# Kernel tuning notes

Measured on AMD Instinct MI355X. Metric: run time of the kernel, lower is better.

## Reference

```python
import jax, jax.numpy as jnp
import numpy as np

NUM_HEADS = 16
HEAD_DIM = 64
HIDDEN = NUM_HEADS * HEAD_DIM  # 1024


def get_rel_pos(q_size, k_size, rel_pos):
    # q_size == k_size here and rel_pos already has 2*size-1 rows, so the
    # F.interpolate(mode='linear') resize in the original is an identity.
    # relative_coords = q - k + (k_size - 1)  (scale factors are 1.0)
    coords = jnp.arange(q_size)[:, None] - jnp.arange(k_size)[None, :] + (k_size - 1)
    return rel_pos[coords]  # [q_size, k_size, head_dim]


def setup_inputs() -> dict:
    key = jax.random.key(0)
    ks = jax.random.split(key, 7)
    B, H, W = 4, 56, 28
    inp = {
        "hidden_states": jax.random.normal(ks[0], (B, H, W, HIDDEN), jnp.float32),
        "qkv_w": jax.random.normal(ks[1], (3 * HIDDEN, HIDDEN), jnp.float32) * 0.02,
        "qkv_b": jax.random.normal(ks[2], (3 * HIDDEN,), jnp.float32) * 0.02,
        "proj_w": jax.random.normal(ks[3], (HIDDEN, HIDDEN), jnp.float32) * 0.02,
        "proj_b": jax.random.normal(ks[4], (HIDDEN,), jnp.float32) * 0.02,
        "rel_pos_h": jax.random.normal(ks[5], (2 * H - 1, HEAD_DIM), jnp.float32) * 0.02,
        "rel_pos_w": jax.random.normal(ks[6], (2 * W - 1, HEAD_DIM), jnp.float32) * 0.02,
    }
    return inp


def reference(hidden_states, qkv_w, qkv_b, proj_w, proj_b, rel_pos_h, rel_pos_w):
    B, H, W, C = hidden_states.shape
    N = H * W
    scale = HEAD_DIM ** -0.5

    # qkv projection -> [3, B*heads, N, head_dim]
    qkv = hidden_states @ qkv_w.T + qkv_b
    qkv = qkv.reshape(B, N, 3, NUM_HEADS, HEAD_DIM).transpose(2, 0, 3, 1, 4)
    qkv = qkv.reshape(3, B * NUM_HEADS, N, HEAD_DIM)
    query, key_, value = qkv[0], qkv[1], qkv[2]

    # scaled dot-product scores, fully materialized as in the original
    attn = jnp.einsum('bqd,bkd->bqk', query * scale, key_)  # [B*heads, N, N]

    # decomposed relative position bias
    Rh = get_rel_pos(H, H, rel_pos_h)  # [H, H, d]
    Rw = get_rel_pos(W, W, rel_pos_w)  # [W, W, d]
    q_r = query.reshape(B * NUM_HEADS, H, W, HEAD_DIM)
    rel_h = jnp.einsum('bhwc,hkc->bhwk', q_r, Rh)  # [B*heads, H, W, H]
    rel_w = jnp.einsum('bhwc,wkc->bhwk', q_r, Rw)  # [B*heads, H, W, W]
    attn = attn.reshape(B * NUM_HEADS, H, W, H, W)
    attn = attn + rel_h[:, :, :, :, None] + rel_w[:, :, :, None, :]
    attn = attn.reshape(B * NUM_HEADS, N, N)

    attn = jax.nn.softmax(attn.astype(jnp.float32), axis=-1).astype(query.dtype)

    out = jnp.einsum('bqk,bkd->bqd', attn, value)
    out = out.reshape(B, NUM_HEADS, H, W, HEAD_DIM).transpose(0, 2, 3, 1, 4)
    out = out.reshape(B, H, W, C)
    out = out @ proj_w.T + proj_b
    return out
```

## Files before the change

### kernel.cpp

```cpp
#include <hip/hip_runtime.h>
#include <hip/hip_bf16.h>
#include <stdint.h>

typedef __bf16 bf16;
typedef __bf16 bf16x2 __attribute__((ext_vector_type(2)));
typedef __bf16 bf16x4 __attribute__((ext_vector_type(4)));
typedef __bf16 bf16x8 __attribute__((ext_vector_type(8)));
typedef float f32x4 __attribute__((ext_vector_type(4)));

#define AS1 __attribute__((address_space(1)))
#define AS3 __attribute__((address_space(3)))

static __device__ __forceinline__ void async_cp16(const bf16* g, bf16* l) {
    __builtin_amdgcn_global_load_lds((const AS1 void*)g, (AS3 void*)l, 16, 0, 0);
}

static __device__ __forceinline__ bf16x4 cvt4(f32x4 v) {
    bf16x4 r;
    r[0] = (bf16)v[0]; r[1] = (bf16)v[1]; r[2] = (bf16)v[2]; r[3] = (bf16)v[3];
    return r;
}

static __device__ __forceinline__ float fast_exp2(float x) {
#if __has_builtin(__builtin_amdgcn_exp2f)
    return __builtin_amdgcn_exp2f(x);
#else
    return __expf(x * 0.69314718056f);
#endif
}

__global__ __launch_bounds__(256) void cvt_kernel(
    const float* __restrict__ src, bf16* __restrict__ dst, int n4) {
    int i = blockIdx.x * 256 + threadIdx.x;
    const int stride = gridDim.x * 256;
    for (; i < n4; i += stride)
        ((bf16x4*)dst)[i] = cvt4(((const f32x4*)src)[i]);
}

__global__ __launch_bounds__(256) void build_kone(bf16* __restrict__ Kone) {
    const int idx = blockIdx.x * 256 + threadIdx.x;
    if (idx >= 6400) return;
    const int key = idx >> 2, chunk = idx & 3;
    const int hk = key / 28;
    const int wk = key - hk * 28;
    const int kt = key >> 6;
    const int ha = (kt << 6) / 28;
    const int jw = 27 - wk;
    const int jh = 31 - (hk - ha);
    bf16x8 v;
#pragma unroll
    for (int e = 0; e < 8; e++) {
        const int j = chunk * 8 + e;
        v[e] = (j == jw || j == jh) ? (bf16)1.0f : (bf16)0.0f;
    }
    *(bf16x8*)&Kone[key * 32 + chunk * 8] = v;
}


#define QKV_EPILOGUE()                                                        \
    for (int nt = 0; nt < 4; nt++) {                                          \
        const int n_ = n0 + wn + nt * 16 + lm;                                \
        const float bv = bias[n_];                                            \
        const int s = n_ >> 10, rem = n_ & 1023;                              \
        const int h = rem >> 6, d = rem & 63;                                 \
        const float qsc = (s == 0) ? 0.18033688011112042f : 1.0f;             \
        for (int mt = 0; mt < 4; mt++) {                                      \
            for (int r = 0; r < 4; r++) {                                     \
                const int m_ = m0 + wm + mt * 16 + quad * 4 + r;              \
                const int b = m_ / 1568;                                      \
                const int pix = m_ - b * 1568;                                \
                const int g = b * 16 + h;                                     \
                const bf16 v = (bf16)((acc[mt][nt][r] + bv) * qsc);           \
                if (s == 0)      Qb[((size_t)g * 1568 + pix) * 64 + d] = v;   \
                else if (s == 1) Kb[((size_t)g * 1568 + pix) * 64 + d] = v;   \
                else {                                                        \
                    const int lk = pix & 31;                                  \
                    const int ppix = (pix & ~31) | ((lk & 15) << 1) | (lk >> 4); \
                    Vt[((size_t)g * 64 + d) * 1568 + ppix] = v;               \
                }                                                             \
            }                                                                 \
        }                                                                     \
    }

__global__ __launch_bounds__(256) void qkv_gemm_bf16(
    const bf16* __restrict__ A, const bf16* __restrict__ W,
    const float* __restrict__ bias, bf16* __restrict__ Qb,
    bf16* __restrict__ Kb, bf16* __restrict__ Vt) {
    __shared__ bf16 As[128 * 32];
    __shared__ bf16 Bs[128 * 32];
    const int t = threadIdx.x;
    const int wid = t >> 6, lane = t & 63;
    const int m0 = blockIdx.x * 128, n0 = blockIdx.y * 128;
    const int wm = (wid & 1) * 64, wn = (wid >> 1) * 64;
    const int r_i = lane >> 2, c8 = (lane & 3) * 8;
    const int lm = lane & 15, quad = lane >> 4;

    f32x4 acc[4][4] = {};
    for (int k0 = 0; k0 < 1024; k0 += 32) {
        __syncthreads();
        for (int i = 0; i < 2; i++) {
            const int blk = wid * 2 + i;
            async_cp16(A + (size_t)(m0 + blk * 16 + r_i) * 1024 + k0 + c8, As + blk * 512);
            async_cp16(W + (size_t)(n0 + blk * 16 + r_i) * 1024 + k0 + c8, Bs + blk * 512);
        }
        __syncthreads();
        bf16x8 af[4], bfr[4];
        for (int x = 0; x < 4; x++) {
            af[x]  = *(const bf16x8*)&As[(wm + x * 16 + lm) * 32 + quad * 8];
            bfr[x] = *(const bf16x8*)&Bs[(wn + x * 16 + lm) * 32 + quad * 8];
        }
        for (int mt = 0; mt < 4; mt++)
            for (int nt = 0; nt < 4; nt++)
                acc[mt][nt] = __builtin_amdgcn_mfma_f32_16x16x32_bf16(af[mt], bfr[nt], acc[mt][nt], 0, 0, 0);
    }
    QKV_EPILOGUE()
}

__global__ __launch_bounds__(256) void qkv_gemm_f32(
    const float* __restrict__ A, const float* __restrict__ W,
    const float* __restrict__ bias, bf16* __restrict__ Qb,
    bf16* __restrict__ Kb, bf16* __restrict__ Vt) {
    __shared__ bf16 As[128 * 32];
    __shared__ bf16 Bs[128 * 32];
    const int t = threadIdx.x;
    const int wid = t >> 6, lane = t & 63;
    const int m0 = blockIdx.x * 128, n0 = blockIdx.y * 128;
    const int wm = (wid & 1) * 64, wn = (wid >> 1) * 64;
    const int lm = lane & 15, quad = lane >> 4;

    f32x4 acc[4][4] = {};
    for (int k0 = 0; k0 < 1024; k0 += 32) {
        __syncthreads();
        for (int i = 0; i < 4; i++) {
            const int idx = t + i * 256;
            const int row = idx >> 3, c4 = (idx & 7) * 4;
            const f32x4 av = *(const f32x4*)&A[(size_t)(m0 + row) * 1024 + k0 + c4];
            const f32x4 wv = *(const f32x4*)&W[(size_t)(n0 + row) * 1024 + k0 + c4];
            *(bf16x4*)&As[row * 32 + c4] = cvt4(av);
            *(bf16x4*)&Bs[row * 32 + c4] = cvt4(wv);
        }
        __syncthreads();
        bf16x8 af[4], bfr[4];
        for (int x = 0; x < 4; x++) {
            af[x]  = *(const bf16x8*)&As[(wm + x * 16 + lm) * 32 + quad * 8];
            bfr[x] = *(const bf16x8*)&Bs[(wn + x * 16 + lm) * 32 + quad * 8];
        }
        for (int mt = 0; mt < 4; mt++)
            for (int nt = 0; nt < 4; nt++)
                acc[mt][nt] = __builtin_amdgcn_mfma_f32_16x16x32_bf16(af[mt], bfr[nt], acc[mt][nt], 0, 0, 0);
    }
    QKV_EPILOGUE()
}

__global__ __launch_bounds__(256) void flash_attn(
    const bf16* __restrict__ Qb, const bf16* __restrict__ Kb,
    const bf16* __restrict__ Vt, const float* __restrict__ rph,
    const float* __restrict__ rpw, const bf16* __restrict__ Kone,
    bf16* __restrict__ AO) {
    const int x = blockIdx.x;
    const int xcd = x & 7, j = x >> 3;
    const int g = xcd * 8 + j / 25;
    const int qblk = j - (j / 25) * 25;
    const int q0 = qblk * 64;
    const int hqb = q0 / 28;

    __shared__ __align__(16) char smem[45312];
    float* Th  = (float*)smem;
    const char* ThC = (const char*)smem;
    bf16* TwS = (bf16*)(smem + 15616);
    char* B   = smem + 19712;
    bf16* Qs  = (bf16*)B;
    bf16* RPs = (bf16*)B;
    float* TwF = (float*)(B + 9216);
    char* KsC = B;
    char* VsC = B + 8192;
    bf16* KoneS = (bf16*)(B + 16384);
    bf16* Ps  = (bf16*)(B + 20480);

    const int t = threadIdx.x, wid = t >> 6, lane = t & 63;
    const int lm = lane & 15, quad = lane >> 4;
    const int qbase_l = wid * 16 + quad * 4;
    const int swz = (lm & 7) << 4;

    for (int c = t; c < 512; c += 256) {
        const int row = c >> 3, col = (c & 7) * 8;
        const int qg = min(q0 + row, 1567);
        *(bf16x8*)&Qs[row * 72 + col] =
            *(const bf16x8*)&Qb[((size_t)g * 1568 + qg) * 64 + col];
    }
    __syncthreads();
    const int qrow_l = wid * 16 + lm;
    const bf16x8 qf0 = *(const bf16x8*)&Qs[qrow_l * 72 + quad * 8];
    const bf16x8 qf1 = *(const bf16x8*)&Qs[qrow_l * 72 + 32 + quad * 8];

    const int qgl = min(q0 + qrow_l, 1567);
    const int thb2 = (qrow_l * 61 + (qgl / 28 - hqb) + 54) * 4;

    const int kobase = ((t >> 2) << 5) + ((t & 3) << 3);
    bf16x8 kreg[2], vreg[2], koreg;
#pragma unroll
    for (int i = 0; i < 2; i++) {
        const int idx = (i << 8) + t;
        kreg[i] = *(const bf16x8*)&Kb[((size_t)g * 1568 + (idx >> 3)) * 64 + ((idx & 7) << 3)];
        vreg[i] = *(const bf16x8*)&Vt[((size_t)g * 64 + (idx >> 3)) * 1568 + ((idx & 7) << 3)];
    }
    koreg = *(const bf16x8*)&Kone[kobase];
    __syncthreads();

    for (int c = t; c < 1024; c += 256) {
        const int row = c >> 4, col = (c & 15) * 4;
        const int rg = min(hqb + row, 110);
        *(bf16x4*)&RPs[row * 72 + col] = cvt4(*(const f32x4*)&rph[rg * 64 + col]);
    }
    __syncthreads();
    f32x4 acch[4];
#pragma unroll
    for (int nt = 0; nt < 4; nt++) {
        const bf16x8 b0 = *(const bf16x8*)&RPs[(nt * 16 + lm) * 72 + quad * 8];
        const bf16x8 b1 = *(const bf16x8*)&RPs[(nt * 16 + lm) * 72 + 32 + quad * 8];
        f32x4 a = {};
        a = __builtin_amdgcn_mfma_f32_16x16x32_bf16(qf0, b0, a, 0, 0, 0);
        a = __builtin_amdgcn_mfma_f32_16x16x32_bf16(qf1, b1, a, 0, 0, 0);
        acch[nt] = a;
    }
    __syncthreads();

    for (int c = t; c < 1024; c += 256) {
        const int row = c >> 4, col = (c & 15) * 4;
        const int rg = min(row, 54);
        *(bf16x4*)&RPs[row * 72 + col] = cvt4(*(const f32x4*)&rpw[rg * 64 + col]);
    }
#pragma unroll
    for (int nt = 0; nt < 4; nt++) {
        const int c = nt * 16 + lm;
        if (c < 59) {
#pragma unroll
            for (int r = 0; r < 4; r++)
                Th[(qbase_l + r) * 61 + c + 2] = acch[nt][r] * 8.0f;
        }
    }
    __syncthreads();
#pragma unroll
    for (int nt = 0; nt < 4; nt++) {
        const bf16x8 b0 = *(const bf16x8*)&RPs[(nt * 16 + lm) * 72 + quad * 8];
        const bf16x8 b1 = *(const bf16x8*)&RPs[(nt * 16 + lm) * 72 + 32 + quad * 8];
        f32x4 a = {};
        a = __builtin_amdgcn_mfma_f32_16x16x32_bf16(qf0, b0, a, 0, 0, 0);
        a = __builtin_amdgcn_mfma_f32_16x16x32_bf16(qf1, b1, a, 0, 0, 0);
        const int c = nt * 16 + lm;
        if (c < 55) {
#pragma unroll
            for (int r = 0; r < 4; r++)
                TwF[(qbase_l + r) * 58 + c] = a[r] * 8.0f;
        }
    }
    __syncthreads();

    {
        const int row = t >> 2, chunk = t & 3;
        const int qg = min(q0 + row, 1567);
        const int wq = qg % 28;
        const float* src = &TwF[row * 58 + wq];
        bf16x8 v;
        if (chunk < 3) {
#pragma unroll
            for (int e = 0; e < 8; e++) v[e] = (bf16)src[chunk * 8 + e];
        } else {
#pragma unroll
            for (int e = 0; e < 4; e++) v[e] = (bf16)src[24 + e];
#pragma unroll
            for (int e = 4; e < 8; e++) v[e] = (bf16)0.0f;
        }
        *(bf16x8*)&TwS[row * 32 + chunk * 8] = v;
    }
    __syncthreads();

    const bf16x8 qt_mine = *(const bf16x8*)&TwS[qrow_l * 32 + quad * 8];

    f32x4 o[4] = {};
    f32x4 lsum = {};
    const f32x4 zero4 = {};
    bf16x8 ones;
#pragma unroll
    for (int i = 0; i < 8; i++) ones[i] = (bf16)1.0f;

    bf16* Pw = &Ps[wid * 640];

    for (int kt = 0; kt < 25; kt++) {
        const int ha = (kt << 6) / 28;
        const char* tp = ThC + (thb2 - (ha << 2));
        const float w0 = *(const float*)(tp);
        const float w1 = *(const float*)(tp + 4);
        const float w2 = *(const float*)(tp + 8);
        const float w3 = *(const float*)(tp + 12);
        bf16x8 qmod = qt_mine;
        qmod[4] = (bf16)w0; qmod[5] = (bf16)w1;
        qmod[6] = (bf16)w2; qmod[7] = (bf16)w3;
        const bf16x8 qf2 = (quad == 3) ? qmod : qt_mine;

        __syncthreads();
#pragma unroll
        for (int i = 0; i < 2; i++) {
            const int idx = (i << 8) + t;
            const int row = idx >> 3;
            const int cb = (((idx & 7) << 4) ^ ((row & 7) << 4));
            *(bf16x8*)(KsC + row * 128 + cb) = kreg[i];
            *(bf16x8*)(VsC + row * 128 + cb) = vreg[i];
        }
        *(bf16x8*)&KoneS[kobase] = koreg;
        {
            const int ktn = min(kt + 1, 24);
            const int kb = ktn << 6;
#pragma unroll
            for (int i = 0; i < 2; i++) {
                const int idx = (i << 8) + t;
                const int krow = min(kb + (idx >> 3), 1567);
                kreg[i] = *(const bf16x8*)&Kb[((size_t)g * 1568 + krow) * 64 + ((idx & 7) << 3)];
                const int vcol = min(kb + ((idx & 7) << 3), 1560);
                vreg[i] = *(const bf16x8*)&Vt[((size_t)g * 64 + (idx >> 3)) * 1568 + vcol];
            }
            koreg = *(const bf16x8*)&Kone[((size_t)ktn << 11) + kobase];
        }
        __syncthreads();

        __builtin_amdgcn_s_setprio(1);
        f32x4 s[4];
#pragma unroll
        for (int f = 0; f < 4; f++) {
            const bf16x8 ko = *(const bf16x8*)&KoneS[(f * 16 + lm) * 32 + quad * 8];
            s[f] = __builtin_amdgcn_mfma_f32_16x16x32_bf16(qf2, ko, zero4, 0, 0, 0);
        }
#pragma unroll
        for (int f = 0; f < 4; f++) {
            const char* rp = KsC + (f * 16 + lm) * 128;
            const int x0 = (quad * 16) ^ swz;
            const bf16x8 ka = *(const bf16x8*)(rp + x0);
            const bf16x8 kb2 = *(const bf16x8*)(rp + (x0 ^ 64));
            s[f] = __builtin_amdgcn_mfma_f32_16x16x32_bf16(qf0, ka, s[f], 0, 0, 0);
            s[f] = __builtin_amdgcn_mfma_f32_16x16x32_bf16(qf1, kb2, s[f], 0, 0, 0);
        }
        __builtin_amdgcn_s_setprio(0);

        if (kt == 24) {
#pragma unroll
            for (int r = 0; r < 4; r++) { s[2][r] = -30000.0f; s[3][r] = -30000.0f; }
        }

#pragma unroll
        for (int h = 0; h < 2; h++) {
#pragma unroll
            for (int r = 0; r < 4; r++) {
                const float p0 = fast_exp2(s[2 * h][r]);
                const float p1 = fast_exp2(s[2 * h + 1][r]);
                bf16x2 pp; pp[0] = (bf16)p0; pp[1] = (bf16)p1;
                *(bf16x2*)&Pw[(quad * 4 + r) * 40 + lm * 2] = pp;
            }
            __asm__ volatile("s_waitcnt lgkmcnt(0)" ::: "memory");
            const bf16x8 pf = *(const bf16x8*)&Pw[lm * 40 + quad * 8];
            lsum = __builtin_amdgcn_mfma_f32_16x16x32_bf16(pf, ones, lsum, 0, 0, 0);
            __builtin_amdgcn_s_setprio(1);
#pragma unroll
            for (int dt = 0; dt < 4; dt++) {
                const bf16x8 vf = *(const bf16x8*)(VsC + (dt * 16 + lm) * 128 +
                                                   (((h << 6) + quad * 16) ^ swz));
                o[dt] = __builtin_amdgcn_mfma_f32_16x16x32_bf16(pf, vf, o[dt], 0, 0, 0);
            }
            __builtin_amdgcn_s_setprio(0);
        }
    }

    if (q0 + wid * 16 < 1568) {
        const int bo = g >> 4, hh = g & 15;
#pragma unroll
        for (int r = 0; r < 4; r++) {
            const float inv = 1.0f / lsum[r];
            const size_t base = ((size_t)bo * 1568 + q0 + qbase_l + r) * 1024 + hh * 64;
#pragma unroll
            for (int dt = 0; dt < 4; dt++)
                AO[base + dt * 16 + lm] = (bf16)(o[dt][r] * inv);
        }
    }
}

__global__ __launch_bounds__(256) void proj_gemm_bf16(
    const bf16* __restrict__ A, const bf16* __restrict__ W,
    const float* __restrict__ bias, float* __restrict__ out) {
    __shared__ bf16 As[128 * 32];
    __shared__ bf16 Bs[128 * 32];
    const int t = threadIdx.x;
    const int wid = t >> 6, lane = t & 63;
    const int m0 = blockIdx.x * 128, n0 = blockIdx.y * 128;
    const int wm = (wid & 1) * 64, wn = (wid >> 1) * 64;
    const int r_i = lane >> 2, c8 = (lane & 3) * 8;
    const int lm = lane & 15, quad = lane >> 4;

    f32x4 acc[4][4] = {};
    for (int k0 = 0; k0 < 1024; k0 += 32) {
        __syncthreads();
        for (int i = 0; i < 2; i++) {
            const int blk = wid * 2 + i;
            async_cp16(A + (size_t)(m0 + blk * 16 + r_i) * 1024 + k0 + c8, As + blk * 512);
            async_cp16(W + (size_t)(n0 + blk * 16 + r_i) * 1024 + k0 + c8, Bs + blk * 512);
        }
        __syncthreads();
        bf16x8 af[4], bfr[4];
        for (int x = 0; x < 4; x++) {
            af[x]  = *(const bf16x8*)&As[(wm + x * 16 + lm) * 32 + quad * 8];
            bfr[x] = *(const bf16x8*)&Bs[(wn + x * 16 + lm) * 32 + quad * 8];
        }
        for (int mt = 0; mt < 4; mt++)
            for (int nt = 0; nt < 4; nt++)
                acc[mt][nt] = __builtin_amdgcn_mfma_f32_16x16x32_bf16(af[mt], bfr[nt], acc[mt][nt], 0, 0, 0);
    }
    for (int nt = 0; nt < 4; nt++) {
        const int n_ = n0 + wn + nt * 16 + lm;
        const float bv = bias[n_];
        for (int mt = 0; mt < 4; mt++)
            for (int r = 0; r < 4; r++) {
                const int m_ = m0 + wm + mt * 16 + quad * 4 + r;
                out[(size_t)m_ * 1024 + n_] = acc[mt][nt][r] + bv;
            }
    }
}

__global__ __launch_bounds__(256) void proj_gemm_f32(
    const bf16* __restrict__ A, const float* __restrict__ W,
    const float* __restrict__ bias, float* __restrict__ out) {
    __shared__ bf16 As[128 * 32];
    __shared__ bf16 Bs[128 * 32];
    const int t = threadIdx.x;
    const int wid = t >> 6, lane = t & 63;
    const int m0 = blockIdx.x * 128, n0 = blockIdx.y * 128;
    const int wm = (wid & 1) * 64, wn = (wid >> 1) * 64;
    const int r_i = lane >> 2, c8 = (lane & 3) * 8;
    const int lm = lane & 15, quad = lane >> 4;

    f32x4 acc[4][4] = {};
    for (int k0 = 0; k0 < 1024; k0 += 32) {
        __syncthreads();
        for (int i = 0; i < 2; i++) {
            const int blk = wid * 2 + i;
            async_cp16(A + (size_t)(m0 + blk * 16 + r_i) * 1024 + k0 + c8, As + blk * 512);
        }
        for (int i = 0; i < 4; i++) {
            const int idx = t + i * 256;
            const int row = idx >> 3, c4 = (idx & 7) * 4;
            const f32x4 wv = *(const f32x4*)&W[(size_t)(n0 + row) * 1024 + k0 + c4];
            *(bf16x4*)&Bs[row * 32 + c4] = cvt4(wv);
        }
        __syncthreads();
        bf16x8 af[4], bfr[4];
        for (int x = 0; x < 4; x++) {
            af[x]  = *(const bf16x8*)&As[(wm + x * 16 + lm) * 32 + quad * 8];
            bfr[x] = *(const bf16x8*)&Bs[(wn + x * 16 + lm) * 32 + quad * 8];
        }
        for (int mt = 0; mt < 4; mt++)
            for (int nt = 0; nt < 4; nt++)
                acc[mt][nt] = __builtin_amdgcn_mfma_f32_16x16x32_bf16(af[mt], bfr[nt], acc[mt][nt], 0, 0, 0);
    }
    for (int nt = 0; nt < 4; nt++) {
        const int n_ = n0 + wn + nt * 16 + lm;
        const float bv = bias[n_];
        for (int mt = 0; mt < 4; mt++)
            for (int r = 0; r < 4; r++) {
                const int m_ = m0 + wm + mt * 16 + quad * 4 + r;
                out[(size_t)m_ * 1024 + n_] = acc[mt][nt][r] + bv;
            }
    }
}

extern "C" void kernel_launch(void* const* d_in, const int* in_sizes, int n_in,
                              void* d_out, int out_size, void* d_ws, size_t ws_size,
                              hipStream_t stream) {
    const float* hs     = (const float*)d_in[0];
    const float* qkv_w  = (const float*)d_in[1];
    const float* qkv_b  = (const float*)d_in[2];
    const float* proj_w = (const float*)d_in[3];
    const float* proj_b = (const float*)d_in[4];
    const float* rph    = (const float*)d_in[5];
    const float* rpw    = (const float*)d_in[6];
    float* out = (float*)d_out;

    const size_t GQ = (size_t)64 * 1568 * 64;
    const size_t N_KONE = (size_t)1600 * 32;
    const size_t N_HS = (size_t)6272 * 1024;
    const size_t N_QW = (size_t)3072 * 1024;
    const size_t N_PW = (size_t)1024 * 1024;
    bf16* Qb = (bf16*)d_ws;
    bf16* Kb = Qb + GQ;
    bf16* Vt = Kb + GQ;
    bf16* AO = Vt + GQ;
    bf16* Kone = AO + GQ;
    bf16* hs_bf    = Kone + N_KONE;
    bf16* qkvw_bf  = hs_bf + N_HS;
    bf16* projw_bf = qkvw_bf + N_QW;
    const size_t need = (4 * GQ + N_KONE + N_HS + N_QW + N_PW) * sizeof(bf16);

    if (ws_size >= need) {
        build_kone<<<25, 256, 0, stream>>>(Kone);
        cvt_kernel<<<512, 256, 0, stream>>>(hs, hs_bf, (int)(N_HS / 4));
        cvt_kernel<<<512, 256, 0, stream>>>(qkv_w, qkvw_bf, (int)(N_QW / 4));
        cvt_kernel<<<256, 256, 0, stream>>>(proj_w, projw_bf, (int)(N_PW / 4));
        qkv_gemm_bf16<<<dim3(49, 24), 256, 0, stream>>>(hs_bf, qkvw_bf, qkv_b, Qb, Kb, Vt);
        flash_attn<<<1600, 256, 0, stream>>>(Qb, Kb, Vt, rph, rpw, Kone, AO);
        proj_gemm_bf16<<<dim3(49, 8), 256, 0, stream>>>(AO, projw_bf, proj_b, out);
    } else {
        build_kone<<<25, 256, 0, stream>>>(Kone);
        qkv_gemm_f32<<<dim3(49, 24), 256, 0, stream>>>(hs, qkv_w, qkv_b, Qb, Kb, Vt);
        flash_attn<<<1600, 256, 0, stream>>>(Qb, Kb, Vt, rph, rpw, Kone, AO);
        proj_gemm_f32<<<dim3(49, 8), 256, 0, stream>>>(AO, proj_w, proj_b, out);
    }
}
```

Measured before the change: 328.3 us.

## Double-buffer K/V tiles in LDS via async global-to-LDS copies in attention

The attention loop now loads K and V tiles straight into a double-buffered LDS area using global_load_lds async copies. This replaces the register-staged load, LDS store and two barriers per iteration with a single barrier. K and V rows are padded to 1600 keys and the pads are zeroed by a new kernel, so the clamped index math goes away. The Kone one-hot fragments are read into registers from global memory rather than LDS, and the rel-pos-h table is stored as bf16 with a 64 stride. The trade-off is more LDS per block (51200 bytes), which may lower occupancy, plus a small extra kernel launch.

```diff
diff --git a/kernel.cpp b/kernel.cpp
--- a/kernel.cpp
+++ b/kernel.cpp
@@ -54,6 +54,20 @@
         v[e] = (j == jw || j == jh) ? (bf16)1.0f : (bf16)0.0f;
     }
     *(bf16x8*)&Kone[key * 32 + chunk * 8] = v;
+}
+
+__global__ __launch_bounds__(256) void zero_pads(
+    bf16* __restrict__ Kb, bf16* __restrict__ Vt) {
+    const int idx = blockIdx.x * 256 + threadIdx.x;
+    if (idx >= 32768) return;
+    const int g = idx >> 9, r = idx & 511;
+    bf16x8 z = {};
+    if (r < 256) {
+        *(bf16x8*)&Kb[((size_t)g * 1600 + 1568) * 64 + r * 8] = z;
+    } else {
+        const int rr = r - 256;
+        *(bf16x8*)&Vt[((size_t)g * 64 + (rr >> 2)) * 1600 + 1568 + (rr & 3) * 8] = z;
+    }
 }
 
 
@@ -72,11 +86,11 @@
                 const int g = b * 16 + h;                                     \
                 const bf16 v = (bf16)((acc[mt][nt][r] + bv) * qsc);           \
                 if (s == 0)      Qb[((size_t)g * 1568 + pix) * 64 + d] = v;   \
-                else if (s == 1) Kb[((size_t)g * 1568 + pix) * 64 + d] = v;   \
+                else if (s == 1) Kb[((size_t)g * 1600 + pix) * 64 + d] = v;   \
                 else {                                                        \
                     const int lk = pix & 31;                                  \
                     const int ppix = (pix & ~31) | ((lk & 15) << 1) | (lk >> 4); \
-                    Vt[((size_t)g * 64 + d) * 1568 + ppix] = v;               \
+                    Vt[((size_t)g * 64 + d) * 1600 + ppix] = v;               \
                 }                                                             \
             }                                                                 \
         }                                                                     \
@@ -164,23 +178,30 @@
     const int q0 = qblk * 64;
     const int hqb = q0 / 28;
 
-    __shared__ __align__(16) char smem[45312];
-    float* Th  = (float*)smem;
+    __shared__ __align__(16) char smem[51200];
+    bf16* Th = (bf16*)smem;
     const char* ThC = (const char*)smem;
-    bf16* TwS = (bf16*)(smem + 15616);
-    char* B   = smem + 19712;
-    bf16* Qs  = (bf16*)B;
-    bf16* RPs = (bf16*)B;
-    float* TwF = (float*)(B + 9216);
-    char* KsC = B;
-    char* VsC = B + 8192;
-    bf16* KoneS = (bf16*)(B + 16384);
-    bf16* Ps  = (bf16*)(B + 20480);
+    char* B = smem + 8192;
+    bf16* Qs  = (bf16*)(B + 32768);
+    bf16* RPh = (bf16*)(B + 0);
+    bf16* RPw = (bf16*)(B + 9216);
+    float* TwF = (float*)(B + 18432);
+    bf16* TwS = (bf16*)(B + 33280);
 
     const int t = threadIdx.x, wid = t >> 6, lane = t & 63;
     const int lm = lane & 15, quad = lane >> 4;
     const int qbase_l = wid * 16 + quad * 4;
     const int swz = (lm & 7) << 4;
+    const int l3 = lane >> 3, l7 = lane & 7;
+    const int swe = ((l7 ^ l3) << 3);
+
+    const bf16* kSrc[2];
+    const bf16* vSrc[2];
+#pragma unroll
+    for (int i = 0; i < 2; i++) {
+        kSrc[i] = Kb + ((size_t)g * 1600 + wid * 16 + i * 8 + l3) * 64 + swe;
+        vSrc[i] = Vt + ((size_t)g * 64 + wid * 16 + i * 8 + l3) * 1600 + swe;
+    }
 
     for (int c = t; c < 512; c += 256) {
         const int row = c >> 3, col = (c & 7) * 8;
@@ -188,36 +209,29 @@
         *(bf16x8*)&Qs[row * 72 + col] =
             *(const bf16x8*)&Qb[((size_t)g * 1568 + qg) * 64 + col];
     }
+    for (int c = t; c < 1024; c += 256) {
+        const int row = c >> 4, col = (c & 15) * 4;
+        const int rg = min(hqb + row, 110);
+        *(bf16x4*)&RPh[row * 72 + col] = cvt4(*(const f32x4*)&rph[rg * 64 + col]);
+    }
     __syncthreads();
+
     const int qrow_l = wid * 16 + lm;
     const bf16x8 qf0 = *(const bf16x8*)&Qs[qrow_l * 72 + quad * 8];
     const bf16x8 qf1 = *(const bf16x8*)&Qs[qrow_l * 72 + 32 + quad * 8];
-
     const int qgl = min(q0 + qrow_l, 1567);
-    const int thb2 = (qrow_l * 61 + (qgl / 28 - hqb) + 54) * 4;
-
-    const int kobase = ((t >> 2) << 5) + ((t & 3) << 3);
-    bf16x8 kreg[2], vreg[2], koreg;
-#pragma unroll
-    for (int i = 0; i < 2; i++) {
-        const int idx = (i << 8) + t;
-        kreg[i] = *(const bf16x8*)&Kb[((size_t)g * 1568 + (idx >> 3)) * 64 + ((idx & 7) << 3)];
-        vreg[i] = *(const bf16x8*)&Vt[((size_t)g * 64 + (idx >> 3)) * 1568 + ((idx & 7) << 3)];
-    }
-    koreg = *(const bf16x8*)&Kone[kobase];
-    __syncthreads();
+    const int thb2 = (qrow_l * 64 + (qgl / 28 - hqb) + 54) * 2;
 
     for (int c = t; c < 1024; c += 256) {
         const int row = c >> 4, col = (c & 15) * 4;
-        const int rg = min(hqb + row, 110);
-        *(bf16x4*)&RPs[row * 72 + col] = cvt4(*(const f32x4*)&rph[rg * 64 + col]);
-    }
-    __syncthreads();
+        const int rg = min(row, 54);
+        *(bf16x4*)&RPw[row * 72 + col] = cvt4(*(const f32x4*)&rpw[rg * 64 + col]);
+    }
     f32x4 acch[4];
 #pragma unroll
     for (int nt = 0; nt < 4; nt++) {
-        const bf16x8 b0 = *(const bf16x8*)&RPs[(nt * 16 + lm) * 72 + quad * 8];
-        const bf16x8 b1 = *(const bf16x8*)&RPs[(nt * 16 + lm) * 72 + 32 + quad * 8];
+        const bf16x8 b0 = *(const bf16x8*)&RPh[(nt * 16 + lm) * 72 + quad * 8];
+        const bf16x8 b1 = *(const bf16x8*)&RPh[(nt * 16 + lm) * 72 + 32 + quad * 8];
         f32x4 a = {};
         a = __builtin_amdgcn_mfma_f32_16x16x32_bf16(qf0, b0, a, 0, 0, 0);
         a = __builtin_amdgcn_mfma_f32_16x16x32_bf16(qf1, b1, a, 0, 0, 0);
@@ -225,25 +239,26 @@
     }
     __syncthreads();
 
-    for (int c = t; c < 1024; c += 256) {
-        const int row = c >> 4, col = (c & 15) * 4;
-        const int rg = min(row, 54);
-        *(bf16x4*)&RPs[row * 72 + col] = cvt4(*(const f32x4*)&rpw[rg * 64 + col]);
-    }
 #pragma unroll
     for (int nt = 0; nt < 4; nt++) {
         const int c = nt * 16 + lm;
         if (c < 59) {
 #pragma unroll
             for (int r = 0; r < 4; r++)
-                Th[(qbase_l + r) * 61 + c + 2] = acch[nt][r] * 8.0f;
-        }
-    }
-    __syncthreads();
+                Th[(qbase_l + r) * 64 + c + 2] = (bf16)(acch[nt][r] * 8.0f);
+        }
+    }
+    if (lm == 0) {
+#pragma unroll
+        for (int r = 0; r < 4; r++) {
+            Th[(qbase_l + r) * 64 + 0] = (bf16)0.0f;
+            Th[(qbase_l + r) * 64 + 1] = (bf16)0.0f;
+        }
+    }
 #pragma unroll
     for (int nt = 0; nt < 4; nt++) {
-        const bf16x8 b0 = *(const bf16x8*)&RPs[(nt * 16 + lm) * 72 + quad * 8];
-        const bf16x8 b1 = *(const bf16x8*)&RPs[(nt * 16 + lm) * 72 + 32 + quad * 8];
+        const bf16x8 b0 = *(const bf16x8*)&RPw[(nt * 16 + lm) * 72 + quad * 8];
+        const bf16x8 b1 = *(const bf16x8*)&RPw[(nt * 16 + lm) * 72 + 32 + quad * 8];
         f32x4 a = {};
         a = __builtin_amdgcn_mfma_f32_16x16x32_bf16(qf0, b0, a, 0, 0, 0);
         a = __builtin_amdgcn_mfma_f32_16x16x32_bf16(qf1, b1, a, 0, 0, 0);
@@ -277,6 +292,19 @@
 
     const bf16x8 qt_mine = *(const bf16x8*)&TwS[qrow_l * 32 + quad * 8];
 
+#pragma unroll
+    for (int i = 0; i < 2; i++) {
+        async_cp16(kSrc[i], (bf16*)(B + (wid * 2 + i) * 1024));
+        async_cp16(vSrc[i], (bf16*)(B + 16384 + (wid * 2 + i) * 1024));
+        kSrc[i] += 4096;
+        vSrc[i] += 64;
+    }
+    const bf16* kop = Kone + lm * 32 + quad * 8;
+    bf16x8 ko[4];
+#pragma unroll
+    for (int f = 0; f < 4; f++) ko[f] = *(const bf16x8*)(kop + f * 512);
+    __syncthreads();
+
     f32x4 o[4] = {};
     f32x4 lsum = {};
     const f32x4 zero4 = {};
@@ -284,88 +312,99 @@
 #pragma unroll
     for (int i = 0; i < 8; i++) ones[i] = (bf16)1.0f;
 
-    bf16* Pw = &Ps[wid * 640];
-
+    bf16* P0w = (bf16*)(B + 32768) + wid * 640;
+    bf16* P1w = (bf16*)(B + 37888) + wid * 640;
+
+    int curo = 0;
     for (int kt = 0; kt < 25; kt++) {
-        const int ha = (kt << 6) / 28;
-        const char* tp = ThC + (thb2 - (ha << 2));
-        const float w0 = *(const float*)(tp);
-        const float w1 = *(const float*)(tp + 4);
-        const float w2 = *(const float*)(tp + 8);
-        const float w3 = *(const float*)(tp + 12);
-        bf16x8 qmod = qt_mine;
-        qmod[4] = (bf16)w0; qmod[5] = (bf16)w1;
-        qmod[6] = (bf16)w2; qmod[7] = (bf16)w3;
-        const bf16x8 qf2 = (quad == 3) ? qmod : qt_mine;
-
-        __syncthreads();
-#pragma unroll
-        for (int i = 0; i < 2; i++) {
-            const int idx = (i << 8) + t;
-            const int row = idx >> 3;
-            const int cb = (((idx & 7) << 4) ^ ((row & 7) << 4));
-            *(bf16x8*)(KsC + row * 128 + cb) = kreg[i];
-            *(bf16x8*)(VsC + row * 128 + cb) = vreg[i];
-        }
-        *(bf16x8*)&KoneS[kobase] = koreg;
-        {
-            const int ktn = min(kt + 1, 24);
-            const int kb = ktn << 6;
+        bf16x8 qf2 = qt_mine;
+        if (quad == 3) {
+            const int ha = (kt << 6) / 28;
+            const char* tp = ThC + (thb2 - (ha << 1));
+            qf2[4] = *(const bf16*)(tp);
+            qf2[5] = *(const bf16*)(tp + 2);
+            qf2[6] = *(const bf16*)(tp + 4);
+            qf2[7] = *(const bf16*)(tp + 6);
+        }
+
+        if (kt < 24) {
+            const int nxto = curo ^ 8192;
 #pragma unroll
             for (int i = 0; i < 2; i++) {
-                const int idx = (i << 8) + t;
-                const int krow = min(kb + (idx >> 3), 1567);
-                kreg[i] = *(const bf16x8*)&Kb[((size_t)g * 1568 + krow) * 64 + ((idx & 7) << 3)];
-                const int vcol = min(kb + ((idx & 7) << 3), 1560);
-                vreg[i] = *(const bf16x8*)&Vt[((size_t)g * 64 + (idx >> 3)) * 1568 + vcol];
+                async_cp16(kSrc[i], (bf16*)(B + nxto + (wid * 2 + i) * 1024));
+                async_cp16(vSrc[i], (bf16*)(B + 16384 + nxto + (wid * 2 + i) * 1024));
+                kSrc[i] += 4096;
+                vSrc[i] += 64;
             }
-            koreg = *(const bf16x8*)&Kone[((size_t)ktn << 11) + kobase];
-        }
-        __syncthreads();
+        }
 
         __builtin_amdgcn_s_setprio(1);
         f32x4 s[4];
 #pragma unroll
-        for (int f = 0; f < 4; f++) {
-            const bf16x8 ko = *(const bf16x8*)&KoneS[(f * 16 + lm) * 32 + quad * 8];
-            s[f] = __builtin_amdgcn_mfma_f32_16x16x32_bf16(qf2, ko, zero4, 0, 0, 0);
-        }
-#pragma unroll
-        for (int f = 0; f < 4; f++) {
-            const char* rp = KsC + (f * 16 + lm) * 128;
+        for (int f = 0; f < 4; f++)
+            s[f] = __builtin_amdgcn_mfma_f32_16x16x32_bf16(qf2, ko[f], zero4, 0, 0, 0);
+        {
+            const char* KsB = B + curo;
             const int x0 = (quad * 16) ^ swz;
-            const bf16x8 ka = *(const bf16x8*)(rp + x0);
-            const bf16x8 kb2 = *(const bf16x8*)(rp + (x0 ^ 64));
-            s[f] = __builtin_amdgcn_mfma_f32_16x16x32_bf16(qf0, ka, s[f], 0, 0, 0);
-            s[f] = __builtin_amdgcn_mfma_f32_16x16x32_bf16(qf1, kb2, s[f], 0, 0, 0);
+#pragma unroll
+            for (int f = 0; f < 4; f++) {
+                const char* rp = KsB + (f * 16 + lm) * 128;
+                const bf16x8 ka = *(const bf16x8*)(rp + x0);
+                const bf16x8 kb2 = *(const bf16x8*)(rp + (x0 ^ 64));
+                s[f] = __builtin_amdgcn_mfma_f32_16x16x32_bf16(qf0, ka, s[f], 0, 0, 0);
+                s[f] = __builtin_amdgcn_mfma_f32_16x16x32_bf16(qf1, kb2, s[f], 0, 0, 0);
+            }
         }
         __builtin_amdgcn_s_setprio(0);
 
+        if (kt < 24) {
+            kop += 2048;
+#pragma unroll
+            for (int f = 0; f < 4; f++) ko[f] = *(const bf16x8*)(kop + f * 512);
+        }
+
         if (kt == 24) {
 #pragma unroll
             for (int r = 0; r < 4; r++) { s[2][r] = -30000.0f; s[3][r] = -30000.0f; }
         }
 
 #pragma unroll
-        for (int h = 0; h < 2; h++) {
-#pragma unroll
-            for (int r = 0; r < 4; r++) {
-                const float p0 = fast_exp2(s[2 * h][r]);
-                const float p1 = fast_exp2(s[2 * h + 1][r]);
-                bf16x2 pp; pp[0] = (bf16)p0; pp[1] = (bf16)p1;
-                *(bf16x2*)&Pw[(quad * 4 + r) * 40 + lm * 2] = pp;
+        for (int r = 0; r < 4; r++) {
+            const float a0 = fast_exp2(s[0][r]);
+            const float a1 = fast_exp2(s[1][r]);
+            bf16x2 pp; pp[0] = (bf16)a0; pp[1] = (bf16)a1;
+            *(bf16x2*)&P0w[(quad * 4 + r) * 40 + lm * 2] = pp;
+            const float b0 = fast_exp2(s[2][r]);
+            const float b1 = fast_exp2(s[3][r]);
+            bf16x2 qq; qq[0] = (bf16)b0; qq[1] = (bf16)b1;
+            *(bf16x2*)&P1w[(quad * 4 + r) * 40 + lm * 2] = qq;
+        }
+        __asm__ volatile("s_waitcnt lgkmcnt(0)" ::: "memory");
+        const bf16x8 pf0 = *(const bf16x8*)&P0w[lm * 40 + quad * 8];
+        const bf16x8 pf1 = *(const bf16x8*)&P1w[lm * 40 + quad * 8];
+        lsum = __builtin_amdgcn_mfma_f32_16x16x32_bf16(pf0, ones, lsum, 0, 0, 0);
+        lsum = __builtin_amdgcn_mfma_f32_16x16x32_bf16(pf1, ones, lsum, 0, 0, 0);
+        __builtin_amdgcn_s_setprio(1);
+        {
+            const char* VsB = B + 16384 + curo;
+#pragma unroll
+            for (int dt = 0; dt < 4; dt++) {
+                const bf16x8 vf = *(const bf16x8*)(VsB + (dt * 16 + lm) * 128 +
+                                                   ((quad * 16) ^ swz));
+                o[dt] = __builtin_amdgcn_mfma_f32_16x16x32_bf16(pf0, vf, o[dt], 0, 0, 0);
             }
-            __asm__ volatile("s_waitcnt lgkmcnt(0)" ::: "memory");
-            const bf16x8 pf = *(const bf16x8*)&Pw[lm * 40 + quad * 8];
-            lsum = __builtin_amdgcn_mfma_f32_16x16x32_bf16(pf, ones, lsum, 0, 0, 0);
-            __builtin_amdgcn_s_setprio(1);
 #pragma unroll
             for (int dt = 0; dt < 4; dt++) {
-                const bf16x8 vf = *(const bf16x8*)(VsC + (dt * 16 + lm) * 128 +
-                                                   (((h << 6) + quad * 16) ^ swz));
-                o[dt] = __builtin_amdgcn_mfma_f32_16x16x32_bf16(pf, vf, o[dt], 0, 0, 0);
+                const bf16x8 vf = *(const bf16x8*)(VsB + (dt * 16 + lm) * 128 +
+                                                   ((64 + quad * 16) ^ swz));
+                o[dt] = __builtin_amdgcn_mfma_f32_16x16x32_bf16(pf1, vf, o[dt], 0, 0, 0);
             }
-            __builtin_amdgcn_s_setprio(0);
+        }
+        __builtin_amdgcn_s_setprio(0);
+
+        if (kt < 24) {
+            __syncthreads();
+            curo ^= 8192;
         }
     }
 
@@ -481,23 +520,25 @@
     const float* rpw    = (const float*)d_in[6];
     float* out = (float*)d_out;
 
-    const size_t GQ = (size_t)64 * 1568 * 64;
+    const size_t GQ  = (size_t)64 * 1568 * 64;
+    const size_t GKP = (size_t)64 * 1600 * 64;
     const size_t N_KONE = (size_t)1600 * 32;
     const size_t N_HS = (size_t)6272 * 1024;
     const size_t N_QW = (size_t)3072 * 1024;
     const size_t N_PW = (size_t)1024 * 1024;
     bf16* Qb = (bf16*)d_ws;
     bf16* Kb = Qb + GQ;
-    bf16* Vt = Kb + GQ;
-    bf16* AO = Vt + GQ;
+    bf16* Vt = Kb + GKP;
+    bf16* AO = Vt + GKP;
     bf16* Kone = AO + GQ;
     bf16* hs_bf    = Kone + N_KONE;
     bf16* qkvw_bf  = hs_bf + N_HS;
     bf16* projw_bf = qkvw_bf + N_QW;
-    const size_t need = (4 * GQ + N_KONE + N_HS + N_QW + N_PW) * sizeof(bf16);
+    const size_t need = (2 * GQ + 2 * GKP + N_KONE + N_HS + N_QW + N_PW) * sizeof(bf16);
 
     if (ws_size >= need) {
         build_kone<<<25, 256, 0, stream>>>(Kone);
+        zero_pads<<<128, 256, 0, stream>>>(Kb, Vt);
         cvt_kernel<<<512, 256, 0, stream>>>(hs, hs_bf, (int)(N_HS / 4));
         cvt_kernel<<<512, 256, 0, stream>>>(qkv_w, qkvw_bf, (int)(N_QW / 4));
         cvt_kernel<<<256, 256, 0, stream>>>(proj_w, projw_bf, (int)(N_PW / 4));
@@ -506,6 +547,7 @@
         proj_gemm_bf16<<<dim3(49, 8), 256, 0, stream>>>(AO, projw_bf, proj_b, out);
     } else {
         build_kone<<<25, 256, 0, stream>>>(Kone);
+        zero_pads<<<128, 256, 0, stream>>>(Kb, Vt);
         qkv_gemm_f32<<<dim3(49, 24), 256, 0, stream>>>(hs, qkv_w, qkv_b, Qb, Kb, Vt);
         flash_attn<<<1600, 256, 0, stream>>>(Qb, Kb, Vt, rph, rpw, Kone, AO);
         proj_gemm_f32<<<dim3(49, 8), 256, 0, stream>>>(AO, proj_w, proj_b, out);
```

Measured after the change: 355.1 us. 8.2% more time.
